# Kernel tuning notes

Measured on AMD Instinct MI355X. Metric: run time of the kernel, lower is better.

## Reference

```python
import jax, jax.numpy as jnp
import numpy as np

UNITS = 64
CHANNEL = 64
L1 = 32
L2 = 32
BATCH = 64


def setup_inputs() -> dict:
    key = jax.random.key(0)
    k1, k2, k3, k4, k5 = jax.random.split(key, 5)
    input_dim = CHANNEL + 3 * UNITS
    inputs = jax.random.normal(k1, (BATCH, CHANNEL, L1, L2), dtype=jnp.float32)
    W = jax.random.normal(k2, (input_dim, UNITS * 7), dtype=jnp.float32) * (1.0 / np.sqrt(input_dim))
    U_rec = jax.random.normal(k3, (UNITS * 3, UNITS), dtype=jnp.float32) * (1.0 / np.sqrt(UNITS * 3))
    bias = jnp.zeros((UNITS * 8,), dtype=jnp.float32)
    W_ij = jax.random.normal(k4, (CHANNEL, UNITS), dtype=jnp.float32) * (1.0 / np.sqrt(CHANNEL))
    return {"inputs": inputs, "W": W, "U_rec": U_rec, "bias": bias, "W_ij": W_ij}


def reference(inputs, W, U_rec, bias, W_ij):
    B, C, l1, l2 = inputs.shape
    u = W_ij.shape[1]
    wr, br = W[:, : 3 * u], bias[: 3 * u]
    wz, bz = W[:, 3 * u : 7 * u], bias[3 * u : 7 * u]
    b_ij = bias[7 * u :]

    # [L1*L2, B, C] scan order: row-major over (i, j), direction 'lt'
    x = jnp.transpose(inputs, (2, 3, 0, 1)).reshape(l1 * l2, B, C)
    states0 = jnp.zeros((l1 + 1, l2 + 1, B, u), dtype=inputs.dtype)  # zero boundary

    def step(carry, xs):
        states, _ = carry
        s_ij, t = xs
        i = t // l2
        j = t % l2
        h_diag = states[i, j]        # [B, u]
        h_top = states[i, j + 1]
        h_left = states[i + 1, j]
        # q = [h_top, h_left, h_diag, s_ij] : [B, 3u + C]
        q = jnp.concatenate([h_top, h_left, h_diag, s_ij], axis=1)
        r = jax.nn.sigmoid(q @ wr + br)                     # [B, 3u]
        z = q @ wz + bz                                     # [B, 4u]
        zg = jax.nn.softmax(z.reshape(B, 4, u), axis=1)     # softmax across 4 gates per unit
        zi, zl, zt, zd = zg[:, 0], zg[:, 1], zg[:, 2], zg[:, 3]
        h_hat = jnp.tanh(
            s_ij @ W_ij + b_ij
            + (r * jnp.concatenate([h_left, h_top, h_diag], axis=1)) @ U_rec
        )
        h_ij = zl * h_left + zt * h_top + zd * h_diag + zi * h_hat
        states = states.at[i + 1, j + 1].set(h_ij)
        return (states, h_ij), None

    tsteps = jnp.arange(l1 * l2)
    (_, h_last), _ = jax.lax.scan(
        step, (states0, jnp.zeros((B, u), dtype=inputs.dtype)), (x, tsteps)
    )
    return h_last
```

## Files before the change

### kernel.cpp

```cpp
#include <hip/hip_runtime.h>
#include <cstdint>
#include <cstddef>


#define LDIM   32
#define BATCH  64
#define UNITS  64
#define CHAN   64
#define NBT    4
#define BT     16
#define TPB    512

typedef _Float16 f16;
typedef _Float16 f16x8 __attribute__((ext_vector_type(8)));
typedef float    f32x4 __attribute__((ext_vector_type(4)));

__global__ __launch_bounds__(TPB, 2) void spatial_gru_kernel(
    const float* __restrict__ x,
    const float* __restrict__ W,
    const float* __restrict__ Urec,
    const float* __restrict__ bias,
    const float* __restrict__ Wij,
    float* __restrict__ out,
    uint32_t* __restrict__ hbuf)
{
    const int p    = blockIdx.x;
    const int xcd  = p & 7;
    const int slot = p >> 3;
    const int row  = xcd * 4 + (slot >> 2);
    const int bt   = slot & 3;
    const int b0   = bt * BT;
    const int t    = (int)threadIdx.x;
    const int u    = t & 63;
    const int g    = t >> 6;
    const int l15  = t & 15;
    const int lq   = (t & 63) >> 4;

    __shared__ __attribute__((aligned(16))) f16 qf[BT][264];
    __shared__ __attribute__((aligned(16))) f16 rf[BT][200];
    __shared__ float qs32[BT][204];
    __shared__ float Gsz [BT][260];
    __shared__ float pacc[4][BT][68];

    f16x8 wreg[4][8];
    float bias1[4] = {0.f, 0.f, 0.f, 0.f};
    if (g < 7) {
        const int nb = g * 64 + l15;
#pragma unroll
        for (int T = 0; T < 4; ++T) {
            bias1[T] = bias[nb + 16 * T];
#pragma unroll
            for (int s = 0; s < 8; ++s) {
                f16x8 v;
#pragma unroll
                for (int jj = 0; jj < 8; ++jj) {
                    int kk = s * 32 + lq * 8 + jj;
                    v[jj] = (f16)W[(size_t)kk * 448 + nb + 16 * T];
                }
                wreg[T][s] = v;
            }
        }
    }
    f16x8 wreg2[4][2];
    {
        const int kb = (g & 3) * 64;
#pragma unroll
        for (int T = 0; T < 4; ++T) {
            const int nn = T * 16 + l15;
#pragma unroll
            for (int s = 0; s < 2; ++s) {
                f16x8 v;
#pragma unroll
                for (int jj = 0; jj < 8; ++jj) {
                    int kk = kb + s * 32 + lq * 8 + jj;
                    float wv = (kk < 192) ? Urec[kk * 64 + nn] : Wij[(kk - 192) * 64 + nn];
                    v[jj] = (f16)wv;
                }
                wreg2[T][s] = v;
            }
        }
    }
    const float bij = bias[448 + u];

    for (int idx = t; idx < 192 * BT; idx += TPB) {
        int b = idx & 15, k = idx >> 4;
        qs32[b][k] = 0.f;
        qf[b][k] = (f16)0.f;
    }

    const size_t xb0 = (size_t)(b0 + g) * 65536 + (size_t)u * 1024 + (size_t)row * 32;
    const size_t xb1 = xb0 + (size_t)8 * 65536;
    {
        float x0 = x[xb0], x1 = x[xb1];
        qf[g][192 + u]     = (f16)x0;
        qf[g + 8][192 + u] = (f16)x1;
    }

    for (int j = 0; j < LDIM; ++j) {
        __syncthreads();

        uint32_t w = 0;
        const uint32_t* sp = hbuf;
        if (row > 0) {
            sp = hbuf + ((((size_t)(row - 1) * LDIM + j) * NBT + bt) << 9) + (g << 6) + u;
            w = __hip_atomic_load(sp, __ATOMIC_RELAXED, __HIP_MEMORY_SCOPE_AGENT);
        }
        float nx0 = 0.f, nx1 = 0.f;
        if (j < LDIM - 1) { nx0 = x[xb0 + j + 1]; nx1 = x[xb1 + j + 1]; }

        f32x4 acc[4];
        if (g < 7) {
#pragma unroll
            for (int T = 0; T < 4; ++T)
                acc[T] = (f32x4){bias1[T], bias1[T], bias1[T], bias1[T]};
#pragma unroll
            for (int s = 2; s < 8; ++s) {
                f16x8 a = *(const f16x8*)&qf[l15][s * 32 + lq * 8];
#pragma unroll
                for (int T = 0; T < 4; ++T)
                    acc[T] = __builtin_amdgcn_mfma_f32_16x16x32_f16(a, wreg[T][s], acc[T], 0, 0, 0);
            }
        } else {
            f32x4 a2[4];
#pragma unroll
            for (int T = 0; T < 4; ++T) a2[T] = (f32x4){0.f, 0.f, 0.f, 0.f};
#pragma unroll
            for (int s = 0; s < 2; ++s) {
                f16x8 a = *(const f16x8*)&qf[l15][192 + s * 32 + lq * 8];
#pragma unroll
                for (int T = 0; T < 4; ++T)
                    a2[T] = __builtin_amdgcn_mfma_f32_16x16x32_f16(a, wreg2[T][s], a2[T], 0, 0, 0);
            }
#pragma unroll
            for (int T = 0; T < 4; ++T)
#pragma unroll
                for (int r = 0; r < 4; ++r)
                    pacc[3][lq * 4 + r][T * 16 + l15] = a2[T][r];
        }

        {
            float ht0 = 0.f, ht1 = 0.f;
            f16 hf0 = (f16)0.f, hf1 = (f16)0.f;
            if (row > 0) {
                while ((w & 0x00010001u) != 0x00010001u) {
                    __builtin_amdgcn_s_sleep(1);
                    w = __hip_atomic_load(sp, __ATOMIC_RELAXED, __HIP_MEMORY_SCOPE_AGENT);
                }
                uint16_t lo = (uint16_t)(w & 0xFFFFu), hi = (uint16_t)(w >> 16);
                hf0 = __builtin_bit_cast(f16, lo);
                hf1 = __builtin_bit_cast(f16, hi);
                ht0 = (float)hf0;
                ht1 = (float)hf1;
            }
            qs32[g][u]     = ht0;  qf[g][u]     = hf0;
            qs32[g + 8][u] = ht1;  qf[g + 8][u] = hf1;
        }
        __syncthreads();

        if (g < 7) {
            {
                f16x8 a0 = *(const f16x8*)&qf[l15][lq * 8];
                f16x8 a1 = *(const f16x8*)&qf[l15][32 + lq * 8];
#pragma unroll
                for (int T = 0; T < 4; ++T)
                    acc[T] = __builtin_amdgcn_mfma_f32_16x16x32_f16(a0, wreg[T][0], acc[T], 0, 0, 0);
#pragma unroll
                for (int T = 0; T < 4; ++T)
                    acc[T] = __builtin_amdgcn_mfma_f32_16x16x32_f16(a1, wreg[T][1], acc[T], 0, 0, 0);
            }
            if (g < 3) {
                const int colbase = (g == 0) ? 64 : (g == 1) ? 0 : 128;
#pragma unroll
                for (int T = 0; T < 4; ++T)
#pragma unroll
                    for (int r = 0; r < 4; ++r) {
                        float rr = 1.f / (1.f + __expf(-acc[T][r]));
                        int b = lq * 4 + r;
                        float hv = qs32[b][colbase + T * 16 + l15];
                        rf[b][g * 64 + T * 16 + l15] = (f16)(rr * hv);
                    }
            } else {
                const int zb = (g - 3) * 64;
#pragma unroll
                for (int T = 0; T < 4; ++T)
#pragma unroll
                    for (int r = 0; r < 4; ++r)
                        Gsz[lq * 4 + r][zb + T * 16 + l15] = acc[T][r];
            }
        }
        __syncthreads();

        if (g >= 4 && g < 7) {
            const int wv = g - 4;
            const int kb = wv * 64;
            f32x4 a2[4];
#pragma unroll
            for (int T = 0; T < 4; ++T) a2[T] = (f32x4){0.f, 0.f, 0.f, 0.f};
#pragma unroll
            for (int s = 0; s < 2; ++s) {
                f16x8 a = *(const f16x8*)&rf[l15][kb + s * 32 + lq * 8];
#pragma unroll
                for (int T = 0; T < 4; ++T)
                    a2[T] = __builtin_amdgcn_mfma_f32_16x16x32_f16(a, wreg2[T][s], a2[T], 0, 0, 0);
            }
#pragma unroll
            for (int T = 0; T < 4; ++T)
#pragma unroll
                for (int r = 0; r < 4; ++r)
                    pacc[wv][lq * 4 + r][T * 16 + l15] = a2[T][r];
        } else if (g < 4) {
#pragma unroll
            for (int i = 0; i < 4; ++i) {
                const int b = g * 4 + i;
                float zi = Gsz[b][u],       zl = Gsz[b][64 + u];
                float zt = Gsz[b][128 + u], zd = Gsz[b][192 + u];
                float hT = qs32[b][u], hL = qs32[b][64 + u], hD = qs32[b][128 + u];
                float mx = fmaxf(fmaxf(zi, zl), fmaxf(zt, zd));
                float ei = __expf(zi - mx), el = __expf(zl - mx);
                float et = __expf(zt - mx), ed = __expf(zd - mx);
                float inv = 1.f / (ei + el + et + ed);
                Gsz[b][u]      = (el * hL + et * hT + ed * hD) * inv;
                Gsz[b][64 + u] = ei * inv;
            }
        }
        __syncthreads();

        float hvv[2], hTv[2];
#pragma unroll
        for (int i = 0; i < 2; ++i) {
            const int b = g + 8 * i;
            float hh = bij + pacc[0][b][u] + pacc[1][b][u] + pacc[2][b][u] + pacc[3][b][u];
            float e2 = __expf(2.f * hh);
            float th = 1.f - 2.f / (e2 + 1.f);
            hvv[i] = Gsz[b][u] + Gsz[b][64 + u] * th;
            hTv[i] = qs32[b][u];
        }
        {
            uint16_t lo = (uint16_t)(__builtin_bit_cast(uint16_t, (f16)hvv[0]) | 1u);
            uint16_t hi = (uint16_t)(__builtin_bit_cast(uint16_t, (f16)hvv[1]) | 1u);
            uint32_t pw = ((uint32_t)hi << 16) | lo;
            __hip_atomic_store(
                hbuf + ((((size_t)row * LDIM + j) * NBT + bt) << 9) + (g << 6) + u,
                pw, __ATOMIC_RELAXED, __HIP_MEMORY_SCOPE_AGENT);
        }
        if (row == LDIM - 1 && j == LDIM - 1) {
            out[(size_t)(b0 + g) * UNITS + u]     = hvv[0];
            out[(size_t)(b0 + g + 8) * UNITS + u] = hvv[1];
        }
#pragma unroll
        for (int i = 0; i < 2; ++i) {
            const int b = g + 8 * i;
            qs32[b][128 + u] = hTv[i];
            qs32[b][64 + u]  = hvv[i];
            qf[b][128 + u] = (f16)hTv[i];
            qf[b][64 + u]  = (f16)hvv[i];
        }
        qf[g][192 + u]     = (f16)nx0;
        qf[g + 8][192 + u] = (f16)nx1;
    }
}

extern "C" void kernel_launch(void* const* d_in, const int* in_sizes, int n_in,
                              void* d_out, int out_size, void* d_ws, size_t ws_size,
                              hipStream_t stream) {
    const float* x    = (const float*)d_in[0];
    const float* W    = (const float*)d_in[1];
    const float* Urec = (const float*)d_in[2];
    const float* bias = (const float*)d_in[3];
    const float* Wij  = (const float*)d_in[4];
    float* out = (float*)d_out;

    uint32_t* hbuf = (uint32_t*)d_ws;

    spatial_gru_kernel<<<LDIM * NBT, TPB, 0, stream>>>(
        x, W, Urec, bias, Wij, out, hbuf);
}
```

Before: 259.4 us.

## Fuse candidate matmul with gate combine and drop a per-step barrier

Waves 4-7 now each compute the full K=256 h_hat product (U_rec plus W_ij) for 16 output columns, using 8 MFMAs in two accumulator chains. The same waves then apply tanh, the softmax gating and the state update, and store the result. This removes the partial-sum buffer and one __syncthreads per recurrence step. The x input slot and the left/diag state columns are double-buffered by step parity so the next step's writes do not race with current reads. Each wave now runs a longer serial MFMA chain, and hbuf is written with 16-bit atomic stores instead of packed 32-bit stores.

```diff
diff --git a/kernel.cpp b/kernel.cpp
--- a/kernel.cpp
+++ b/kernel.cpp
@@ -36,11 +36,10 @@
     const int l15  = t & 15;
     const int lq   = (t & 63) >> 4;
 
-    __shared__ __attribute__((aligned(16))) f16 qf[BT][264];
+    __shared__ __attribute__((aligned(16))) f16 qf[BT][328];
     __shared__ __attribute__((aligned(16))) f16 rf[BT][200];
-    __shared__ float qs32[BT][204];
+    __shared__ float qs32[BT][324];
     __shared__ float Gsz [BT][260];
-    __shared__ float pacc[4][BT][68];
 
     f16x8 wreg[4][8];
     float bias1[4] = {0.f, 0.f, 0.f, 0.f};
@@ -61,30 +60,28 @@
             }
         }
     }
-    f16x8 wreg2[4][2];
-    {
-        const int kb = (g & 3) * 64;
-#pragma unroll
-        for (int T = 0; T < 4; ++T) {
-            const int nn = T * 16 + l15;
-#pragma unroll
-            for (int s = 0; s < 2; ++s) {
-                f16x8 v;
-#pragma unroll
-                for (int jj = 0; jj < 8; ++jj) {
-                    int kk = kb + s * 32 + lq * 8 + jj;
-                    float wv = (kk < 192) ? Urec[kk * 64 + nn] : Wij[(kk - 192) * 64 + nn];
-                    v[jj] = (f16)wv;
-                }
-                wreg2[T][s] = v;
-            }
-        }
-    }
-    const float bij = bias[448 + u];
-
+    f16x8 wreg2[8];
+    float bijE = 0.f;
+    if (g >= 4) {
+        const int nn = (g - 4) * 16 + l15;
+        bijE = bias[448 + nn];
+#pragma unroll
+        for (int s = 0; s < 8; ++s) {
+            f16x8 v;
+#pragma unroll
+            for (int jj = 0; jj < 8; ++jj) {
+                int kk = s * 32 + lq * 8 + jj;
+                float wv = (kk < 192) ? Urec[kk * 64 + nn] : Wij[(kk - 192) * 64 + nn];
+                v[jj] = (f16)wv;
+            }
+            wreg2[s] = v;
+        }
+    }
+
+    for (int idx = t; idx < BT * 324; idx += TPB)
+        ((float*)qs32)[idx] = 0.f;
     for (int idx = t; idx < 192 * BT; idx += TPB) {
         int b = idx & 15, k = idx >> 4;
-        qs32[b][k] = 0.f;
         qf[b][k] = (f16)0.f;
     }
 
@@ -97,13 +94,19 @@
     }
 
     for (int j = 0; j < LDIM; ++j) {
+        const int par  = j & 1;
+        const int scur = 192 + par * 64;
+        const int snxt = 192 + (par ^ 1) * 64;
+        const int hlc  = 64 + par * 128, hdc = 128 + par * 128;
+        const int hln  = 64 + (par ^ 1) * 128, hdn = 128 + (par ^ 1) * 128;
+
         __syncthreads();
 
-        uint32_t w = 0;
+        uint32_t wv_ = 0;
         const uint32_t* sp = hbuf;
         if (row > 0) {
             sp = hbuf + ((((size_t)(row - 1) * LDIM + j) * NBT + bt) << 9) + (g << 6) + u;
-            w = __hip_atomic_load(sp, __ATOMIC_RELAXED, __HIP_MEMORY_SCOPE_AGENT);
+            wv_ = __hip_atomic_load(sp, __ATOMIC_RELAXED, __HIP_MEMORY_SCOPE_AGENT);
         }
         float nx0 = 0.f, nx1 = 0.f;
         if (j < LDIM - 1) { nx0 = x[xb0 + j + 1]; nx1 = x[xb1 + j + 1]; }
@@ -115,38 +118,24 @@
                 acc[T] = (f32x4){bias1[T], bias1[T], bias1[T], bias1[T]};
 #pragma unroll
             for (int s = 2; s < 8; ++s) {
-                f16x8 a = *(const f16x8*)&qf[l15][s * 32 + lq * 8];
+                const f16* ap = (s < 6) ? &qf[l15][s * 32 + lq * 8]
+                                        : &qf[l15][scur + (s - 6) * 32 + lq * 8];
+                f16x8 a = *(const f16x8*)ap;
 #pragma unroll
                 for (int T = 0; T < 4; ++T)
                     acc[T] = __builtin_amdgcn_mfma_f32_16x16x32_f16(a, wreg[T][s], acc[T], 0, 0, 0);
             }
-        } else {
-            f32x4 a2[4];
-#pragma unroll
-            for (int T = 0; T < 4; ++T) a2[T] = (f32x4){0.f, 0.f, 0.f, 0.f};
-#pragma unroll
-            for (int s = 0; s < 2; ++s) {
-                f16x8 a = *(const f16x8*)&qf[l15][192 + s * 32 + lq * 8];
-#pragma unroll
-                for (int T = 0; T < 4; ++T)
-                    a2[T] = __builtin_amdgcn_mfma_f32_16x16x32_f16(a, wreg2[T][s], a2[T], 0, 0, 0);
-            }
-#pragma unroll
-            for (int T = 0; T < 4; ++T)
-#pragma unroll
-                for (int r = 0; r < 4; ++r)
-                    pacc[3][lq * 4 + r][T * 16 + l15] = a2[T][r];
         }
 
         {
             float ht0 = 0.f, ht1 = 0.f;
             f16 hf0 = (f16)0.f, hf1 = (f16)0.f;
             if (row > 0) {
-                while ((w & 0x00010001u) != 0x00010001u) {
+                while ((wv_ & 0x00010001u) != 0x00010001u) {
                     __builtin_amdgcn_s_sleep(1);
-                    w = __hip_atomic_load(sp, __ATOMIC_RELAXED, __HIP_MEMORY_SCOPE_AGENT);
+                    wv_ = __hip_atomic_load(sp, __ATOMIC_RELAXED, __HIP_MEMORY_SCOPE_AGENT);
                 }
-                uint16_t lo = (uint16_t)(w & 0xFFFFu), hi = (uint16_t)(w >> 16);
+                uint16_t lo = (uint16_t)(wv_ & 0xFFFFu), hi = (uint16_t)(wv_ >> 16);
                 hf0 = __builtin_bit_cast(f16, lo);
                 hf1 = __builtin_bit_cast(f16, hi);
                 ht0 = (float)hf0;
@@ -169,7 +158,7 @@
                     acc[T] = __builtin_amdgcn_mfma_f32_16x16x32_f16(a1, wreg[T][1], acc[T], 0, 0, 0);
             }
             if (g < 3) {
-                const int colbase = (g == 0) ? 64 : (g == 1) ? 0 : 128;
+                const int colbase = (g == 0) ? hlc : (g == 1) ? 0 : hdc;
 #pragma unroll
                 for (int T = 0; T < 4; ++T)
 #pragma unroll
@@ -190,73 +179,54 @@
         }
         __syncthreads();
 
-        if (g >= 4 && g < 7) {
-            const int wv = g - 4;
-            const int kb = wv * 64;
-            f32x4 a2[4];
-#pragma unroll
-            for (int T = 0; T < 4; ++T) a2[T] = (f32x4){0.f, 0.f, 0.f, 0.f};
-#pragma unroll
-            for (int s = 0; s < 2; ++s) {
-                f16x8 a = *(const f16x8*)&rf[l15][kb + s * 32 + lq * 8];
-#pragma unroll
-                for (int T = 0; T < 4; ++T)
-                    a2[T] = __builtin_amdgcn_mfma_f32_16x16x32_f16(a, wreg2[T][s], a2[T], 0, 0, 0);
-            }
-#pragma unroll
-            for (int T = 0; T < 4; ++T)
-#pragma unroll
-                for (int r = 0; r < 4; ++r)
-                    pacc[wv][lq * 4 + r][T * 16 + l15] = a2[T][r];
-        } else if (g < 4) {
-#pragma unroll
-            for (int i = 0; i < 4; ++i) {
-                const int b = g * 4 + i;
-                float zi = Gsz[b][u],       zl = Gsz[b][64 + u];
-                float zt = Gsz[b][128 + u], zd = Gsz[b][192 + u];
-                float hT = qs32[b][u], hL = qs32[b][64 + u], hD = qs32[b][128 + u];
+        if (g >= 4) {
+            f32x4 aA = (f32x4){0.f, 0.f, 0.f, 0.f};
+            f32x4 aB = (f32x4){0.f, 0.f, 0.f, 0.f};
+#pragma unroll
+            for (int s = 0; s < 8; s += 2) {
+                const f16* apA = (s < 6) ? &rf[l15][s * 32 + lq * 8]
+                                         : &qf[l15][scur + (s - 6) * 32 + lq * 8];
+                f16x8 a = *(const f16x8*)apA;
+                aA = __builtin_amdgcn_mfma_f32_16x16x32_f16(a, wreg2[s], aA, 0, 0, 0);
+                const f16* apB = (s + 1 < 6) ? &rf[l15][(s + 1) * 32 + lq * 8]
+                                             : &qf[l15][scur + (s + 1 - 6) * 32 + lq * 8];
+                f16x8 b_ = *(const f16x8*)apB;
+                aB = __builtin_amdgcn_mfma_f32_16x16x32_f16(b_, wreg2[s + 1], aB, 0, 0, 0);
+            }
+            const int n = (g - 4) * 16 + l15;
+            uint16_t* hp = (uint16_t*)(hbuf + ((((size_t)row * LDIM + j) * NBT + bt) << 9));
+#pragma unroll
+            for (int rr = 0; rr < 4; ++rr) {
+                const int b = lq * 4 + rr;
+                float hh = bijE + aA[rr] + aB[rr];
+                float e2 = __expf(2.f * hh);
+                float th = 1.f - 2.f / (e2 + 1.f);
+                float zi = Gsz[b][n],       zl = Gsz[b][64 + n];
+                float zt = Gsz[b][128 + n], zd = Gsz[b][192 + n];
+                float hT = qs32[b][n], hL = qs32[b][hlc + n], hD = qs32[b][hdc + n];
                 float mx = fmaxf(fmaxf(zi, zl), fmaxf(zt, zd));
                 float ei = __expf(zi - mx), el = __expf(zl - mx);
                 float et = __expf(zt - mx), ed = __expf(zd - mx);
                 float inv = 1.f / (ei + el + et + ed);
-                Gsz[b][u]      = (el * hL + et * hT + ed * hD) * inv;
-                Gsz[b][64 + u] = ei * inv;
-            }
-        }
-        __syncthreads();
-
-        float hvv[2], hTv[2];
-#pragma unroll
-        for (int i = 0; i < 2; ++i) {
-            const int b = g + 8 * i;
-            float hh = bij + pacc[0][b][u] + pacc[1][b][u] + pacc[2][b][u] + pacc[3][b][u];
-            float e2 = __expf(2.f * hh);
-            float th = 1.f - 2.f / (e2 + 1.f);
-            hvv[i] = Gsz[b][u] + Gsz[b][64 + u] * th;
-            hTv[i] = qs32[b][u];
-        }
-        {
-            uint16_t lo = (uint16_t)(__builtin_bit_cast(uint16_t, (f16)hvv[0]) | 1u);
-            uint16_t hi = (uint16_t)(__builtin_bit_cast(uint16_t, (f16)hvv[1]) | 1u);
-            uint32_t pw = ((uint32_t)hi << 16) | lo;
-            __hip_atomic_store(
-                hbuf + ((((size_t)row * LDIM + j) * NBT + bt) << 9) + (g << 6) + u,
-                pw, __ATOMIC_RELAXED, __HIP_MEMORY_SCOPE_AGENT);
-        }
-        if (row == LDIM - 1 && j == LDIM - 1) {
-            out[(size_t)(b0 + g) * UNITS + u]     = hvv[0];
-            out[(size_t)(b0 + g + 8) * UNITS + u] = hvv[1];
-        }
-#pragma unroll
-        for (int i = 0; i < 2; ++i) {
-            const int b = g + 8 * i;
-            qs32[b][128 + u] = hTv[i];
-            qs32[b][64 + u]  = hvv[i];
-            qf[b][128 + u] = (f16)hTv[i];
-            qf[b][64 + u]  = (f16)hvv[i];
-        }
-        qf[g][192 + u]     = (f16)nx0;
-        qf[g + 8][192 + u] = (f16)nx1;
+                float h = (el * hL + et * hT + ed * hD + ei * th) * inv;
+                uint16_t hv16 = (uint16_t)(__builtin_bit_cast(uint16_t, (f16)h) | 1u);
+                __hip_atomic_store(hp + ((((b & 7) << 6) + n) << 1) + (b >> 3),
+                                   hv16, __ATOMIC_RELAXED, __HIP_MEMORY_SCOPE_AGENT);
+                qs32[b][hln + n] = h;
+                qf[b][64 + n]    = (f16)h;
+                if (row == LDIM - 1 && j == LDIM - 1)
+                    out[(size_t)(b0 + b) * UNITS + n] = h;
+            }
+        } else {
+#pragma unroll
+            for (int i = 0; i < 4; ++i) {
+                const int b = g + 4 * i;
+                qs32[b][hdn + u] = qs32[b][u];
+                qf[b][128 + u]   = qf[b][u];
+            }
+        }
+        qf[g][snxt + u]     = (f16)nx0;
+        qf[g + 8][snxt + u] = (f16)nx1;
     }
 }
 
```

Result: slower. 282.6 us (+8.9%).
